# Kernel optimization log

Measured on AMD Instinct MI355X. Metric: run time of the kernel, lower is better.

## Reference

```python
import jax, jax.numpy as jnp
import numpy as np

B, CW_DIM = 256, 8192
DIM_EMBED = 128
DICT_SIZE = 4096
DIM_CODES = CW_DIM // DIM_EMBED  # 64


def setup_inputs() -> dict:
    key = jax.random.key(0)
    k1, k2 = jax.random.split(key)
    x = jax.random.normal(k1, (B, CW_DIM), dtype=jnp.float32)
    dictionary = jax.random.normal(k2, (DIM_CODES, DICT_SIZE, DIM_EMBED), dtype=jnp.float32)
    return {"x": x, "dictionary": dictionary}


def reference(x, dictionary):
    """VQVAE.quantise (eval mode): pairwise sq-distance -> argmin -> gather + one-hot.

    x: [B, cw_dim], dictionary: [C, S, E] with cw_dim = C*E.
    Returns (cw_embed [B, C*E], one_hot_idx [B, C, S]).
    """
    Bb, D = x.shape
    C, S, E = dictionary.shape
    xr = x.reshape(Bb, C, E)                                   # [B, C, E]
    x_sq = jnp.sum(xr * xr, axis=-1, keepdims=True)            # [B, C, 1]
    d_sq = jnp.sum(dictionary * dictionary, axis=-1)           # [C, S]
    cross = jnp.einsum('bce,cse->bcs', xr, dictionary)         # [B, C, S] (GEMM)
    dist = x_sq + d_sq[None, :, :] - 2.0 * cross               # [B, C, S]
    idx = jnp.argmin(dist, axis=-1)                            # [B, C]
    # gather nearest codes: dictionary[c, idx[b,c]] -> [B, C, E]
    code_ids = jnp.arange(C)[None, :]                          # [1, C]
    cw_embed = dictionary[code_ids, idx]                       # [B, C, E]
    cw_embed = cw_embed.reshape(Bb, C * E)                     # [B, cw_dim]
    one_hot_idx = jax.nn.one_hot(idx, S, dtype=x.dtype)        # [B, C, S]
    return cw_embed, one_hot_idx
```

## Files before the change

kernel.cpp:

```cpp
#include <hip/hip_runtime.h>
#include <stdint.h>


#define B_SZ 256
#define C_SZ 64
#define E_SZ 128
#define S_SZ 4096
#define CW   8192
#define LDB  136

typedef __attribute__((ext_vector_type(4))) float    float4a;
typedef __attribute__((ext_vector_type(8))) _Float16 half8;

__device__ __forceinline__ void split8(float4a f0, float4a f1, half8& hi, half8& lo) {
    #pragma unroll
    for (int j = 0; j < 4; ++j) {
        _Float16 h0 = (_Float16)f0[j];
        hi[j]     = h0;
        lo[j]     = (_Float16)(f0[j] - (float)h0);
        _Float16 h1 = (_Float16)f1[j];
        hi[4 + j] = h1;
        lo[4 + j] = (_Float16)(f1[j] - (float)h1);
    }
}

__global__ __launch_bounds__(512, 2) void argmin_mfma(
    const float* __restrict__ x,
    const float* __restrict__ dict,
    int* __restrict__ idx_out,
    float* __restrict__ cw_out)
{
    __shared__ __attribute__((aligned(16))) _Float16 bh[128 * LDB];
    __shared__ __attribute__((aligned(16))) _Float16 bl[128 * LDB];
    __shared__ float4a dsqp[128];
    __shared__ int     fid[64];
    float* rv = reinterpret_cast<float*>(bh);
    int*   ri = reinterpret_cast<int*>(bl);

    const int tid   = threadIdx.x;
    const int lane  = tid & 63;
    const int quad  = lane >> 4;
    const int l15   = lane & 15;
    const int wid   = tid >> 6;
    const int mhalf = wid & 1;
    const int nquad = wid >> 1;
    const int c     = blockIdx.x & 63;
    const int btile = blockIdx.x >> 6;

    int m_attr[4], n_attr[4];
    {
        half8 ones, enc;
        #pragma unroll
        for (int j = 0; j < 8; ++j) { ones[j] = (_Float16)1.0f; enc[j] = (_Float16)(float)l15; }
        float4a z = {0.f, 0.f, 0.f, 0.f};
        float4a pr = __builtin_amdgcn_mfma_f32_16x16x32_f16(enc, ones, z, 0, 0, 0);
        float4a pc = __builtin_amdgcn_mfma_f32_16x16x32_f16(ones, enc, z, 0, 0, 0);
        #pragma unroll
        for (int r = 0; r < 4; ++r) {
            m_attr[r] = (int)(pr[r] * 0.03125f + 0.5f);
            n_attr[r] = (int)(pc[r] * 0.03125f + 0.5f);
        }
    }

    half8 ah[2][4], al[2][4];
    #pragma unroll
    for (int mi = 0; mi < 2; ++mi) {
        int b = btile * 64 + mhalf * 32 + mi * 16 + l15;
        const float* xr = x + (size_t)b * CW + c * E_SZ;
        #pragma unroll
        for (int kk = 0; kk < 4; ++kk) {
            float4a f0 = *reinterpret_cast<const float4a*>(xr + kk * 32 + quad * 8);
            float4a f1 = *reinterpret_cast<const float4a*>(xr + kk * 32 + quad * 8 + 4);
            split8(f0, f1, ah[mi][kk], al[mi][kk]);
        }
    }

    float bestv[8];
    int   besti[8];
    #pragma unroll
    for (int i = 0; i < 8; ++i) { bestv[i] = 3.4e38f; besti[i] = 0; }

    for (int s0 = 0; s0 < S_SZ; s0 += 128) {
        __syncthreads();
        {
            int srow = tid >> 2;
            int kq   = (tid & 3) * 32;
            const float* dr = dict + ((size_t)c * S_SZ + (s0 + srow)) * E_SZ + kq;
            float dp = 0.f;
            #pragma unroll
            for (int ck = 0; ck < 4; ++ck) {
                float4a f0 = *reinterpret_cast<const float4a*>(dr + ck * 8);
                float4a f1 = *reinterpret_cast<const float4a*>(dr + ck * 8 + 4);
                half8 h, l;
                split8(f0, f1, h, l);
                #pragma unroll
                for (int j = 0; j < 4; ++j) { dp = fmaf(f0[j], f0[j], dp); dp = fmaf(f1[j], f1[j], dp); }
                *reinterpret_cast<half8*>(bh + srow * LDB + kq + ck * 8) = h;
                *reinterpret_cast<half8*>(bl + srow * LDB + kq + ck * 8) = l;
            }
            dsqp[srow][tid & 3] = dp;
        }
        __syncthreads();

        half8 bhf[2][4], blf[2][4];
        #pragma unroll
        for (int ni = 0; ni < 2; ++ni) {
            int sl = nquad * 32 + ni * 16 + l15;
            #pragma unroll
            for (int kk = 0; kk < 4; ++kk) {
                bhf[ni][kk] = *reinterpret_cast<const half8*>(bh + sl * LDB + kk * 32 + quad * 8);
                blf[ni][kk] = *reinterpret_cast<const half8*>(bl + sl * LDB + kk * 32 + quad * 8);
            }
        }

        float4a acc[2][2] = {{{0.f,0.f,0.f,0.f},{0.f,0.f,0.f,0.f}},
                             {{0.f,0.f,0.f,0.f},{0.f,0.f,0.f,0.f}}};
        #pragma unroll
        for (int kk = 0; kk < 4; ++kk)
            #pragma unroll
            for (int mi = 0; mi < 2; ++mi)
                #pragma unroll
                for (int ni = 0; ni < 2; ++ni) {
                    acc[mi][ni] = __builtin_amdgcn_mfma_f32_16x16x32_f16(
                        ah[mi][kk], bhf[ni][kk], acc[mi][ni], 0, 0, 0);
                    acc[mi][ni] = __builtin_amdgcn_mfma_f32_16x16x32_f16(
                        ah[mi][kk], blf[ni][kk], acc[mi][ni], 0, 0, 0);
                    acc[mi][ni] = __builtin_amdgcn_mfma_f32_16x16x32_f16(
                        al[mi][kk], bhf[ni][kk], acc[mi][ni], 0, 0, 0);
                }

        #pragma unroll
        for (int ni = 0; ni < 2; ++ni)
            #pragma unroll
            for (int r = 0; r < 4; ++r) {
                int sl = nquad * 32 + ni * 16 + n_attr[r];
                float4a q4 = dsqp[sl];
                float dsq = (q4[0] + q4[1]) + (q4[2] + q4[3]);
                int sg = s0 + sl;
                #pragma unroll
                for (int mi = 0; mi < 2; ++mi) {
                    float dist = dsq - 2.0f * acc[mi][ni][r];
                    int slot = mi * 4 + r;
                    if (dist < bestv[slot]) { bestv[slot] = dist; besti[slot] = sg; }
                }
            }
    }

    __syncthreads();

    #pragma unroll
    for (int mi = 0; mi < 2; ++mi)
        #pragma unroll
        for (int r = 0; r < 4; ++r) {
            int row = mhalf * 32 + mi * 16 + m_attr[r];
            int col = nquad * 16 + n_attr[r];
            rv[row * 64 + col] = bestv[mi * 4 + r];
            ri[row * 64 + col] = besti[mi * 4 + r];
        }
    __syncthreads();

    if (tid < 64) {
        float bv = 3.4e38f; int bi = 0x7fffffff;
        for (int j = 0; j < 64; ++j) {
            float v = rv[tid * 64 + j];
            int   i = ri[tid * 64 + j];
            if (v < bv || (v == bv && i < bi)) { bv = v; bi = i; }
        }
        idx_out[(btile * 64 + tid) * C_SZ + c] = bi;
        fid[tid] = bi;
    }
    __syncthreads();

    for (int u = tid; u < 64 * 32; u += 512) {
        int row = u >> 5, ch = u & 31;
        int bi = fid[row];
        float4a v = *reinterpret_cast<const float4a*>(
            dict + ((size_t)c * S_SZ + bi) * E_SZ + ch * 4);
        *reinterpret_cast<float4a*>(
            cw_out + (size_t)(btile * 64 + row) * CW + c * E_SZ + ch * 4) = v;
    }
}

__global__ void scatter_ones(const int* __restrict__ idx, float* __restrict__ oh) {
    int r = blockIdx.x * 256 + threadIdx.x;
    oh[(size_t)r * S_SZ + idx[r]] = 1.0f;
}

extern "C" void kernel_launch(void* const* d_in, const int* in_sizes, int n_in,
                              void* d_out, int out_size, void* d_ws, size_t ws_size,
                              hipStream_t stream) {
    const float* x    = (const float*)d_in[0];
    const float* dict = (const float*)d_in[1];
    float* out = (float*)d_out;
    int* idx = (int*)d_ws;
    float* oh = out + (size_t)B_SZ * CW;

    hipMemsetAsync(oh, 0, (size_t)B_SZ * C_SZ * S_SZ * sizeof(float), stream);
    argmin_mfma<<<dim3(256), dim3(512), 0, stream>>>(x, dict, idx, out);
    scatter_ones<<<dim3(B_SZ * C_SZ / 256), dim3(256), 0, stream>>>(idx, oh);
}
```

Baseline: 485.2 us.

## Precompute split fp16 dictionary and norms, retile argmin, write one-hot directly

A separate pass converts the fp32 dictionary once into hi/lo fp16 halves plus per-code squared norms. The scratch space for this is the one-hot output region, which is overwritten later. The argmin kernel then loads B fragments straight from global memory, with no per-tile LDS staging or barriers, and uses 256-thread blocks over 32 batch rows, giving twice as many blocks. The memset plus scatter is replaced by one kernel that writes the full one-hot tensor with non-temporal float4 stores. Costs are an extra full-dictionary read/write pass and more redundant global fragment loads across batch tiles.

```diff
diff --git a/kernel.cpp b/kernel.cpp
--- a/kernel.cpp
+++ b/kernel.cpp
@@ -7,7 +7,6 @@
 #define E_SZ 128
 #define S_SZ 4096
 #define CW   8192
-#define LDB  136
 
 typedef __attribute__((ext_vector_type(4))) float    float4a;
 typedef __attribute__((ext_vector_type(8))) _Float16 half8;
@@ -24,26 +23,57 @@
     }
 }
 
-__global__ __launch_bounds__(512, 2) void argmin_mfma(
+__global__ __launch_bounds__(256) void convert_dict(
+    const float* __restrict__ dict,
+    _Float16* __restrict__ dh, _Float16* __restrict__ dl,
+    float* __restrict__ dsq)
+{
+    __shared__ float part[256];
+    const int tid = threadIdx.x;
+    const int r   = tid >> 4;
+    const int ck  = tid & 15;
+    const size_t base = (size_t)blockIdx.x * 2048;
+    const size_t off  = base + (size_t)r * E_SZ + ck * 8;
+
+    float4a f0 = *reinterpret_cast<const float4a*>(dict + off);
+    float4a f1 = *reinterpret_cast<const float4a*>(dict + off + 4);
+    half8 h, l;
+    split8(f0, f1, h, l);
+    *reinterpret_cast<half8*>(dh + off) = h;
+    *reinterpret_cast<half8*>(dl + off) = l;
+
+    float p = 0.f;
+    #pragma unroll
+    for (int j = 0; j < 4; ++j) { p = fmaf(f0[j], f0[j], p); p = fmaf(f1[j], f1[j], p); }
+    part[tid] = p;
+    __syncthreads();
+    if (ck == 0) {
+        float a = 0.f;
+        #pragma unroll
+        for (int j = 0; j < 16; ++j) a += part[r * 16 + j];
+        dsq[blockIdx.x * 16 + r] = a;
+    }
+}
+
+__global__ __launch_bounds__(256) void argmin_mfma2(
     const float* __restrict__ x,
+    const _Float16* __restrict__ dh,
+    const _Float16* __restrict__ dl,
+    const float* __restrict__ dsq_g,
     const float* __restrict__ dict,
     int* __restrict__ idx_out,
     float* __restrict__ cw_out)
 {
-    __shared__ __attribute__((aligned(16))) _Float16 bh[128 * LDB];
-    __shared__ __attribute__((aligned(16))) _Float16 bl[128 * LDB];
-    __shared__ float4a dsqp[128];
-    __shared__ int     fid[64];
-    float* rv = reinterpret_cast<float*>(bh);
-    int*   ri = reinterpret_cast<int*>(bl);
+    __shared__ float s_dsq[S_SZ];
+    __shared__ float rv[32 * 64];
+    __shared__ int   ri[32 * 64];
+    __shared__ int   fid[32];
 
     const int tid   = threadIdx.x;
     const int lane  = tid & 63;
     const int quad  = lane >> 4;
     const int l15   = lane & 15;
-    const int wid   = tid >> 6;
-    const int mhalf = wid & 1;
-    const int nquad = wid >> 1;
+    const int nquad = tid >> 6;
     const int c     = blockIdx.x & 63;
     const int btile = blockIdx.x >> 6;
 
@@ -62,10 +92,17 @@
         }
     }
 
+    {
+        const float4a* src = reinterpret_cast<const float4a*>(dsq_g + c * S_SZ);
+        float4a* dst = reinterpret_cast<float4a*>(s_dsq);
+        #pragma unroll
+        for (int i = 0; i < 4; ++i) dst[tid + i * 256] = src[tid + i * 256];
+    }
+
     half8 ah[2][4], al[2][4];
     #pragma unroll
     for (int mi = 0; mi < 2; ++mi) {
-        int b = btile * 64 + mhalf * 32 + mi * 16 + l15;
+        int b = btile * 32 + mi * 16 + l15;
         const float* xr = x + (size_t)b * CW + c * E_SZ;
         #pragma unroll
         for (int kk = 0; kk < 4; ++kk) {
@@ -74,6 +111,7 @@
             split8(f0, f1, ah[mi][kk], al[mi][kk]);
         }
     }
+    __syncthreads();
 
     float bestv[8];
     int   besti[8];
@@ -81,35 +119,15 @@
     for (int i = 0; i < 8; ++i) { bestv[i] = 3.4e38f; besti[i] = 0; }
 
     for (int s0 = 0; s0 < S_SZ; s0 += 128) {
-        __syncthreads();
-        {
-            int srow = tid >> 2;
-            int kq   = (tid & 3) * 32;
-            const float* dr = dict + ((size_t)c * S_SZ + (s0 + srow)) * E_SZ + kq;
-            float dp = 0.f;
-            #pragma unroll
-            for (int ck = 0; ck < 4; ++ck) {
-                float4a f0 = *reinterpret_cast<const float4a*>(dr + ck * 8);
-                float4a f1 = *reinterpret_cast<const float4a*>(dr + ck * 8 + 4);
-                half8 h, l;
-                split8(f0, f1, h, l);
-                #pragma unroll
-                for (int j = 0; j < 4; ++j) { dp = fmaf(f0[j], f0[j], dp); dp = fmaf(f1[j], f1[j], dp); }
-                *reinterpret_cast<half8*>(bh + srow * LDB + kq + ck * 8) = h;
-                *reinterpret_cast<half8*>(bl + srow * LDB + kq + ck * 8) = l;
-            }
-            dsqp[srow][tid & 3] = dp;
-        }
-        __syncthreads();
-
         half8 bhf[2][4], blf[2][4];
         #pragma unroll
         for (int ni = 0; ni < 2; ++ni) {
             int sl = nquad * 32 + ni * 16 + l15;
+            size_t row = ((size_t)c * S_SZ + s0 + sl) * E_SZ;
             #pragma unroll
             for (int kk = 0; kk < 4; ++kk) {
-                bhf[ni][kk] = *reinterpret_cast<const half8*>(bh + sl * LDB + kk * 32 + quad * 8);
-                blf[ni][kk] = *reinterpret_cast<const half8*>(bl + sl * LDB + kk * 32 + quad * 8);
+                bhf[ni][kk] = *reinterpret_cast<const half8*>(dh + row + kk * 32 + quad * 8);
+                blf[ni][kk] = *reinterpret_cast<const half8*>(dl + row + kk * 32 + quad * 8);
             }
         }
 
@@ -134,8 +152,7 @@
             #pragma unroll
             for (int r = 0; r < 4; ++r) {
                 int sl = nquad * 32 + ni * 16 + n_attr[r];
-                float4a q4 = dsqp[sl];
-                float dsq = (q4[0] + q4[1]) + (q4[2] + q4[3]);
+                float dsq = s_dsq[s0 + sl];
                 int sg = s0 + sl;
                 #pragma unroll
                 for (int mi = 0; mi < 2; ++mi) {
@@ -146,44 +163,54 @@
             }
     }
 
-    __syncthreads();
-
     #pragma unroll
     for (int mi = 0; mi < 2; ++mi)
         #pragma unroll
         for (int r = 0; r < 4; ++r) {
-            int row = mhalf * 32 + mi * 16 + m_attr[r];
+            int row = mi * 16 + m_attr[r];
             int col = nquad * 16 + n_attr[r];
             rv[row * 64 + col] = bestv[mi * 4 + r];
             ri[row * 64 + col] = besti[mi * 4 + r];
         }
     __syncthreads();
 
-    if (tid < 64) {
+    if (tid < 32) {
         float bv = 3.4e38f; int bi = 0x7fffffff;
         for (int j = 0; j < 64; ++j) {
             float v = rv[tid * 64 + j];
             int   i = ri[tid * 64 + j];
             if (v < bv || (v == bv && i < bi)) { bv = v; bi = i; }
         }
-        idx_out[(btile * 64 + tid) * C_SZ + c] = bi;
+        idx_out[(btile * 32 + tid) * C_SZ + c] = bi;
         fid[tid] = bi;
     }
     __syncthreads();
 
-    for (int u = tid; u < 64 * 32; u += 512) {
+    #pragma unroll
+    for (int u = tid; u < 32 * 32; u += 256) {
         int row = u >> 5, ch = u & 31;
         int bi = fid[row];
         float4a v = *reinterpret_cast<const float4a*>(
             dict + ((size_t)c * S_SZ + bi) * E_SZ + ch * 4);
         *reinterpret_cast<float4a*>(
-            cw_out + (size_t)(btile * 64 + row) * CW + c * E_SZ + ch * 4) = v;
-    }
-}
-
-__global__ void scatter_ones(const int* __restrict__ idx, float* __restrict__ oh) {
-    int r = blockIdx.x * 256 + threadIdx.x;
-    oh[(size_t)r * S_SZ + idx[r]] = 1.0f;
+            cw_out + (size_t)(btile * 32 + row) * CW + c * E_SZ + ch * 4) = v;
+    }
+}
+
+__global__ __launch_bounds__(256) void onehot_nt(const int* __restrict__ idx,
+                                                 float* __restrict__ oh) {
+    const unsigned t = blockIdx.x * 256 + threadIdx.x;
+    #pragma unroll
+    for (int i = 0; i < 4; ++i) {
+        unsigned q = t + (unsigned)i * 4194304u;
+        unsigned row = q >> 10;
+        int target = idx[row];
+        unsigned sbase = (q & 1023u) * 4u;
+        float4a v = {0.f, 0.f, 0.f, 0.f};
+        unsigned d = (unsigned)(target - (int)sbase);
+        if (d < 4u) v[d] = 1.0f;
+        __builtin_nontemporal_store(v, reinterpret_cast<float4a*>(oh) + q);
+    }
 }
 
 extern "C" void kernel_launch(void* const* d_in, const int* in_sizes, int n_in,
@@ -195,7 +222,12 @@
     int* idx = (int*)d_ws;
     float* oh = out + (size_t)B_SZ * CW;
 
-    hipMemsetAsync(oh, 0, (size_t)B_SZ * C_SZ * S_SZ * sizeof(float), stream);
-    argmin_mfma<<<dim3(256), dim3(512), 0, stream>>>(x, dict, idx, out);
-    scatter_ones<<<dim3(B_SZ * C_SZ / 256), dim3(256), 0, stream>>>(idx, oh);
-}
+    char* scr = (char*)oh;
+    _Float16* dh  = (_Float16*)scr;
+    _Float16* dl  = (_Float16*)(scr + 67108864);
+    float*    dsq = (float*)   (scr + 134217728);
+
+    convert_dict<<<dim3(16384), dim3(256), 0, stream>>>(dict, dh, dl, dsq);
+    argmin_mfma2<<<dim3(512), dim3(256), 0, stream>>>(x, dh, dl, dsq, dict, idx, out);
+    onehot_nt<<<dim3(16384), dim3(256), 0, stream>>>(idx, oh);
+}
```

Result: slower. 523.8 us (+8.0%).
